# Kernel tuning notes

Measured on AMD Instinct MI355X. Metric: run time of the kernel, lower is better.

Reference implementation:

```python
import jax, jax.numpy as jnp
import numpy as np

N_NODES = 100000
N_EDGES = 600000
D_FEAT = 128
D_DOT = 4


def setup_inputs() -> dict:
    key = jax.random.key(0)
    k1, k2, k3, k4, k5 = jax.random.split(key, 5)
    n = jax.random.normal(k1, (N_NODES, D_FEAT), dtype=jnp.float32)
    e = jax.random.normal(k2, (N_EDGES, D_FEAT), dtype=jnp.float32)
    # xavier_uniform for Linear(D_FEAT, D_DOT); bias filled with 0
    limit = float(np.sqrt(6.0 / (D_FEAT + D_DOT)))
    W = jax.random.uniform(k3, (D_DOT, D_FEAT), dtype=jnp.float32, minval=-limit, maxval=limit)
    b = jnp.zeros((D_DOT,), dtype=jnp.float32)
    src_idx = jax.random.randint(k4, (N_EDGES,), 0, N_NODES, dtype=jnp.int64)
    dst_idx = jax.random.randint(k5, (N_EDGES,), 0, N_NODES, dtype=jnp.int64)
    return {"n": n, "e": e, "W": W, "b": b, "src_idx": src_idx, "dst_idx": dst_idx}


def reference(n, e, W, b, src_idx, dst_idx):
    # gather per-edge src/dst node features: [E, D]
    src = n[src_idx]
    dst = n[dst_idx]
    # include_edge_features=True: mean of node and edge features
    src = (src + e) * 0.5
    dst = (dst + e) * 0.5
    # tiny linear projection to dot_product_dim=4: [E, 4]
    hs = src @ W.T + b
    hd = dst @ W.T + b
    # per-edge dot product (bmm of [E,1,4] x [E,4,1] -> [E,1]) then sigmoid
    score = jax.nn.sigmoid(jnp.sum(hs * hd, axis=-1, keepdims=True))
    return score
```

## Files before the change

### kernel.cpp

```cpp
#include <hip/hip_runtime.h>
#include <math.h>

#define D_FEAT 128
#define D_DOT  4


__device__ __forceinline__ float dot4(const float4 a, const float4 b) {
    return a.x * b.x + a.y * b.y + a.z * b.z + a.w * b.w;
}

template <int CTRL>
__device__ __forceinline__ float dpp_add(float x) {
    union { float f; int i; } u, v;
    u.f = x;
    v.i = __builtin_amdgcn_update_dpp(u.i, u.i, CTRL, 0xF, 0xF, true);
    return x + v.f;
}

__device__ __forceinline__ float row_reduce16(float x) {
    x = dpp_add<0x128>(x);
    x = dpp_add<0x124>(x);
    x = dpp_add<0x122>(x);
    x = dpp_add<0x121>(x);
    return x;
}

__global__ __launch_bounds__(256, 4) void node_proj_kernel(
    const float* __restrict__ n,
    const float* __restrict__ W,
    float* __restrict__ pn,
    int n_nodes)
{
    const int t    = threadIdx.x;
    const int lane = t & 63;
    const int sub  = lane & 15;
    const int g    = lane >> 4;
    const int wave = t >> 6;
    const int base = blockIdx.x * 48 + wave * 12;
    const int last = n_nodes - 1;

    int r[3], c[3];
#pragma unroll
    for (int i = 0; i < 3; ++i) {
        r[i] = base + i * 4 + g;
        c[i] = r[i] > last ? last : r[i];
    }

    const float4* n4 = reinterpret_cast<const float4*>(n);
    float4 xl[3], xh[3];
#pragma unroll
    for (int i = 0; i < 3; ++i) {
        xl[i] = n4[(size_t)c[i] * 32 + sub];
        xh[i] = n4[(size_t)c[i] * 32 + sub + 16];
    }

    const float4* W4 = reinterpret_cast<const float4*>(W);
    float4 wlo[D_DOT], whi[D_DOT];
#pragma unroll
    for (int k = 0; k < D_DOT; ++k) {
        wlo[k] = W4[k * 32 + sub];
        whi[k] = W4[k * 32 + sub + 16];
    }

    float a[3][D_DOT];
#pragma unroll
    for (int i = 0; i < 3; ++i)
#pragma unroll
        for (int k = 0; k < D_DOT; ++k)
            a[i][k] = dot4(xl[i], wlo[k]) + dot4(xh[i], whi[k]);

#pragma unroll
    for (int i = 0; i < 3; ++i)
#pragma unroll
        for (int k = 0; k < D_DOT; ++k)
            a[i][k] = row_reduce16(a[i][k]);

#pragma unroll
    for (int i = 0; i < 3; ++i)
        if (sub == 0 && r[i] < n_nodes)
            reinterpret_cast<float4*>(pn)[r[i]] =
                make_float4(a[i][0], a[i][1], a[i][2], a[i][3]);
}

__global__ __launch_bounds__(256, 4) void edge_score_kernel(
    const float* __restrict__ e,
    const float* __restrict__ W,
    const float* __restrict__ bias,
    const float* __restrict__ pn,
    const int* __restrict__ src_idx,
    const int* __restrict__ dst_idx,
    float* __restrict__ out,
    int n_edges)
{
    const int t    = threadIdx.x;
    const int lane = t & 63;
    const int sub  = lane & 15;
    const int g    = lane >> 4;
    const int wave = t >> 6;
    const int base = blockIdx.x * 48 + wave * 12;
    const int last = n_edges - 1;

    int r[3], c[3];
#pragma unroll
    for (int i = 0; i < 3; ++i) {
        r[i] = base + i * 4 + g;
        c[i] = r[i] > last ? last : r[i];
    }

    int sI[3], dI[3];
#pragma unroll
    for (int i = 0; i < 3; ++i) { sI[i] = src_idx[c[i]]; dI[i] = dst_idx[c[i]]; }

    const float4* e4 = reinterpret_cast<const float4*>(e);
    float4 xl[3], xh[3];
#pragma unroll
    for (int i = 0; i < 3; ++i) {
        xl[i] = e4[(size_t)c[i] * 32 + sub];
        xh[i] = e4[(size_t)c[i] * 32 + sub + 16];
    }

    const float4* W4 = reinterpret_cast<const float4*>(W);
    float4 wlo[D_DOT], whi[D_DOT];
#pragma unroll
    for (int k = 0; k < D_DOT; ++k) {
        wlo[k] = W4[k * 32 + sub];
        whi[k] = W4[k * 32 + sub + 16];
    }
    const float b0 = bias[0], b1 = bias[1], b2 = bias[2], b3 = bias[3];

    const float4* pn4 = reinterpret_cast<const float4*>(pn);
    float4 ps[3], pd[3];
#pragma unroll
    for (int i = 0; i < 3; ++i) { ps[i] = pn4[sI[i]]; pd[i] = pn4[dI[i]]; }

    float a[3][D_DOT];
#pragma unroll
    for (int i = 0; i < 3; ++i)
#pragma unroll
        for (int k = 0; k < D_DOT; ++k)
            a[i][k] = dot4(xl[i], wlo[k]) + dot4(xh[i], whi[k]);

#pragma unroll
    for (int i = 0; i < 3; ++i)
#pragma unroll
        for (int k = 0; k < D_DOT; ++k)
            a[i][k] = row_reduce16(a[i][k]);

#pragma unroll
    for (int i = 0; i < 3; ++i) {
        const float u0 = 0.5f * a[i][0] + b0, u1 = 0.5f * a[i][1] + b1;
        const float u2 = 0.5f * a[i][2] + b2, u3 = 0.5f * a[i][3] + b3;
        const float dot = (0.5f * ps[i].x + u0) * (0.5f * pd[i].x + u0)
                        + (0.5f * ps[i].y + u1) * (0.5f * pd[i].y + u1)
                        + (0.5f * ps[i].z + u2) * (0.5f * pd[i].z + u2)
                        + (0.5f * ps[i].w + u3) * (0.5f * pd[i].w + u3);
        if (sub == 0 && r[i] < n_edges)
            out[r[i]] = 1.0f / (1.0f + __expf(-dot));
    }
}

extern "C" void kernel_launch(void* const* d_in, const int* in_sizes, int n_in,
                              void* d_out, int out_size, void* d_ws, size_t ws_size,
                              hipStream_t stream) {
    const float* n    = (const float*)d_in[0];
    const float* e    = (const float*)d_in[1];
    const float* W    = (const float*)d_in[2];
    const float* bias = (const float*)d_in[3];
    const int*   src  = (const int*)d_in[4];
    const int*   dst  = (const int*)d_in[5];
    float* out = (float*)d_out;

    const int n_nodes = in_sizes[0] / D_FEAT;
    const int n_edges = in_sizes[1] / D_FEAT;

    float* pn = (float*)d_ws;

    const int nblk = (n_nodes + 47) / 48;
    const int eblk = (n_edges + 47) / 48;
    node_proj_kernel<<<nblk, 256, 0, stream>>>(n, W, pn, n_nodes);
    edge_score_kernel<<<eblk, 256, 0, stream>>>(e, W, bias, pn, src, dst, out, n_edges);
}
```

Baseline: 77.78 us.

## Fuse node projection and edge scoring into one cooperative persistent kernel

Replaces the two launches with one cooperative kernel of fixed grid size. It runs grid-stride loops over nodes and then edges, separated by a grid-wide sync, and loads W and bias once per thread. The aim is to remove the second launch and per-block weight reloads. In exchange it adds grid-sync cost and fixes the grid at 1024 blocks, which may underfill or serialize work. It falls back to the old two-kernel path if the cooperative launch fails.

```diff
diff --git a/kernel.cpp b/kernel.cpp
--- a/kernel.cpp
+++ b/kernel.cpp
@@ -1,8 +1,13 @@
 #include <hip/hip_runtime.h>
+#include <hip/hip_cooperative_groups.h>
 #include <math.h>
+
+namespace cg = cooperative_groups;
 
 #define D_FEAT 128
 #define D_DOT  4
+#define NBLK   1024
+#define RPB    48
 
 
 __device__ __forceinline__ float dot4(const float4 a, const float4 b) {
@@ -25,27 +30,136 @@
     return x;
 }
 
-__global__ __launch_bounds__(256, 4) void node_proj_kernel(
+__global__ __launch_bounds__(256, 4) void fused_kernel(
     const float* __restrict__ n,
+    const float* __restrict__ e,
     const float* __restrict__ W,
+    const float* __restrict__ bias,
+    const int* __restrict__ src_idx,
+    const int* __restrict__ dst_idx,
+    float* __restrict__ out,
     float* __restrict__ pn,
-    int n_nodes)
+    int n_nodes, int n_edges)
 {
     const int t    = threadIdx.x;
     const int lane = t & 63;
     const int sub  = lane & 15;
     const int g    = lane >> 4;
     const int wave = t >> 6;
-    const int base = blockIdx.x * 48 + wave * 12;
+
+    const float4* W4 = reinterpret_cast<const float4*>(W);
+    float4 wlo[D_DOT], whi[D_DOT];
+#pragma unroll
+    for (int k = 0; k < D_DOT; ++k) {
+        wlo[k] = W4[k * 32 + sub];
+        whi[k] = W4[k * 32 + sub + 16];
+    }
+    const float b0 = bias[0], b1 = bias[1], b2 = bias[2], b3 = bias[3];
+
+    const int wave_start = blockIdx.x * RPB + wave * 12;
+    const int stride = gridDim.x * RPB;
+
+    {
+        const int last = n_nodes - 1;
+        const float4* n4 = reinterpret_cast<const float4*>(n);
+        for (int base = wave_start; base < n_nodes; base += stride) {
+            int r[3], c[3];
+#pragma unroll
+            for (int i = 0; i < 3; ++i) {
+                r[i] = base + i * 4 + g;
+                c[i] = r[i] > last ? last : r[i];
+            }
+            float4 xl[3], xh[3];
+#pragma unroll
+            for (int i = 0; i < 3; ++i) {
+                xl[i] = n4[(size_t)c[i] * 32 + sub];
+                xh[i] = n4[(size_t)c[i] * 32 + sub + 16];
+            }
+            float a[3][D_DOT];
+#pragma unroll
+            for (int i = 0; i < 3; ++i)
+#pragma unroll
+                for (int k = 0; k < D_DOT; ++k)
+                    a[i][k] = dot4(xl[i], wlo[k]) + dot4(xh[i], whi[k]);
+#pragma unroll
+            for (int i = 0; i < 3; ++i)
+#pragma unroll
+                for (int k = 0; k < D_DOT; ++k)
+                    a[i][k] = row_reduce16(a[i][k]);
+#pragma unroll
+            for (int i = 0; i < 3; ++i)
+                if (sub == 0 && r[i] < n_nodes)
+                    reinterpret_cast<float4*>(pn)[r[i]] =
+                        make_float4(a[i][0], a[i][1], a[i][2], a[i][3]);
+        }
+    }
+
+    __threadfence();
+    cg::this_grid().sync();
+
+    {
+        const int last = n_edges - 1;
+        const float4* e4  = reinterpret_cast<const float4*>(e);
+        const float4* pn4 = reinterpret_cast<const float4*>(pn);
+        for (int base = wave_start; base < n_edges; base += stride) {
+            int r[3], c[3];
+#pragma unroll
+            for (int i = 0; i < 3; ++i) {
+                r[i] = base + i * 4 + g;
+                c[i] = r[i] > last ? last : r[i];
+            }
+            int sI[3], dI[3];
+#pragma unroll
+            for (int i = 0; i < 3; ++i) { sI[i] = src_idx[c[i]]; dI[i] = dst_idx[c[i]]; }
+
+            float4 xl[3], xh[3];
+#pragma unroll
+            for (int i = 0; i < 3; ++i) {
+                xl[i] = e4[(size_t)c[i] * 32 + sub];
+                xh[i] = e4[(size_t)c[i] * 32 + sub + 16];
+            }
+            float4 ps[3], pd[3];
+#pragma unroll
+            for (int i = 0; i < 3; ++i) { ps[i] = pn4[sI[i]]; pd[i] = pn4[dI[i]]; }
+
+            float a[3][D_DOT];
+#pragma unroll
+            for (int i = 0; i < 3; ++i)
+#pragma unroll
+                for (int k = 0; k < D_DOT; ++k)
+                    a[i][k] = dot4(xl[i], wlo[k]) + dot4(xh[i], whi[k]);
+#pragma unroll
+            for (int i = 0; i < 3; ++i)
+#pragma unroll
+                for (int k = 0; k < D_DOT; ++k)
+                    a[i][k] = row_reduce16(a[i][k]);
+
+#pragma unroll
+            for (int i = 0; i < 3; ++i) {
+                const float u0 = 0.5f * a[i][0] + b0, u1 = 0.5f * a[i][1] + b1;
+                const float u2 = 0.5f * a[i][2] + b2, u3 = 0.5f * a[i][3] + b3;
+                const float dot = (0.5f * ps[i].x + u0) * (0.5f * pd[i].x + u0)
+                                + (0.5f * ps[i].y + u1) * (0.5f * pd[i].y + u1)
+                                + (0.5f * ps[i].z + u2) * (0.5f * pd[i].z + u2)
+                                + (0.5f * ps[i].w + u3) * (0.5f * pd[i].w + u3);
+                if (sub == 0 && r[i] < n_edges)
+                    out[r[i]] = 1.0f / (1.0f + __expf(-dot));
+            }
+        }
+    }
+}
+
+__global__ __launch_bounds__(256, 4) void node_proj_kernel(
+    const float* __restrict__ n, const float* __restrict__ W,
+    float* __restrict__ pn, int n_nodes)
+{
+    const int t = threadIdx.x, lane = t & 63, sub = lane & 15, g = lane >> 4;
+    const int wave = t >> 6;
+    const int base = blockIdx.x * RPB + wave * 12;
     const int last = n_nodes - 1;
-
     int r[3], c[3];
 #pragma unroll
-    for (int i = 0; i < 3; ++i) {
-        r[i] = base + i * 4 + g;
-        c[i] = r[i] > last ? last : r[i];
-    }
-
+    for (int i = 0; i < 3; ++i) { r[i] = base + i * 4 + g; c[i] = r[i] > last ? last : r[i]; }
     const float4* n4 = reinterpret_cast<const float4*>(n);
     float4 xl[3], xh[3];
 #pragma unroll
@@ -53,64 +167,43 @@
         xl[i] = n4[(size_t)c[i] * 32 + sub];
         xh[i] = n4[(size_t)c[i] * 32 + sub + 16];
     }
-
     const float4* W4 = reinterpret_cast<const float4*>(W);
     float4 wlo[D_DOT], whi[D_DOT];
 #pragma unroll
-    for (int k = 0; k < D_DOT; ++k) {
-        wlo[k] = W4[k * 32 + sub];
-        whi[k] = W4[k * 32 + sub + 16];
-    }
-
+    for (int k = 0; k < D_DOT; ++k) { wlo[k] = W4[k * 32 + sub]; whi[k] = W4[k * 32 + sub + 16]; }
     float a[3][D_DOT];
 #pragma unroll
     for (int i = 0; i < 3; ++i)
 #pragma unroll
         for (int k = 0; k < D_DOT; ++k)
             a[i][k] = dot4(xl[i], wlo[k]) + dot4(xh[i], whi[k]);
-
 #pragma unroll
     for (int i = 0; i < 3; ++i)
 #pragma unroll
         for (int k = 0; k < D_DOT; ++k)
             a[i][k] = row_reduce16(a[i][k]);
-
 #pragma unroll
     for (int i = 0; i < 3; ++i)
         if (sub == 0 && r[i] < n_nodes)
-            reinterpret_cast<float4*>(pn)[r[i]] =
-                make_float4(a[i][0], a[i][1], a[i][2], a[i][3]);
+            reinterpret_cast<float4*>(pn)[r[i]] = make_float4(a[i][0], a[i][1], a[i][2], a[i][3]);
 }
 
 __global__ __launch_bounds__(256, 4) void edge_score_kernel(
-    const float* __restrict__ e,
-    const float* __restrict__ W,
-    const float* __restrict__ bias,
-    const float* __restrict__ pn,
-    const int* __restrict__ src_idx,
-    const int* __restrict__ dst_idx,
-    float* __restrict__ out,
-    int n_edges)
+    const float* __restrict__ e, const float* __restrict__ W,
+    const float* __restrict__ bias, const float* __restrict__ pn,
+    const int* __restrict__ src_idx, const int* __restrict__ dst_idx,
+    float* __restrict__ out, int n_edges)
 {
-    const int t    = threadIdx.x;
-    const int lane = t & 63;
-    const int sub  = lane & 15;
-    const int g    = lane >> 4;
+    const int t = threadIdx.x, lane = t & 63, sub = lane & 15, g = lane >> 4;
     const int wave = t >> 6;
-    const int base = blockIdx.x * 48 + wave * 12;
+    const int base = blockIdx.x * RPB + wave * 12;
     const int last = n_edges - 1;
-
     int r[3], c[3];
 #pragma unroll
-    for (int i = 0; i < 3; ++i) {
-        r[i] = base + i * 4 + g;
-        c[i] = r[i] > last ? last : r[i];
-    }
-
+    for (int i = 0; i < 3; ++i) { r[i] = base + i * 4 + g; c[i] = r[i] > last ? last : r[i]; }
     int sI[3], dI[3];
 #pragma unroll
     for (int i = 0; i < 3; ++i) { sI[i] = src_idx[c[i]]; dI[i] = dst_idx[c[i]]; }
-
     const float4* e4 = reinterpret_cast<const float4*>(e);
     float4 xl[3], xh[3];
 #pragma unroll
@@ -118,34 +211,26 @@
         xl[i] = e4[(size_t)c[i] * 32 + sub];
         xh[i] = e4[(size_t)c[i] * 32 + sub + 16];
     }
-
     const float4* W4 = reinterpret_cast<const float4*>(W);
     float4 wlo[D_DOT], whi[D_DOT];
 #pragma unroll
-    for (int k = 0; k < D_DOT; ++k) {
-        wlo[k] = W4[k * 32 + sub];
-        whi[k] = W4[k * 32 + sub + 16];
-    }
+    for (int k = 0; k < D_DOT; ++k) { wlo[k] = W4[k * 32 + sub]; whi[k] = W4[k * 32 + sub + 16]; }
     const float b0 = bias[0], b1 = bias[1], b2 = bias[2], b3 = bias[3];
-
     const float4* pn4 = reinterpret_cast<const float4*>(pn);
     float4 ps[3], pd[3];
 #pragma unroll
     for (int i = 0; i < 3; ++i) { ps[i] = pn4[sI[i]]; pd[i] = pn4[dI[i]]; }
-
     float a[3][D_DOT];
 #pragma unroll
     for (int i = 0; i < 3; ++i)
 #pragma unroll
         for (int k = 0; k < D_DOT; ++k)
             a[i][k] = dot4(xl[i], wlo[k]) + dot4(xh[i], whi[k]);
-
 #pragma unroll
     for (int i = 0; i < 3; ++i)
 #pragma unroll
         for (int k = 0; k < D_DOT; ++k)
             a[i][k] = row_reduce16(a[i][k]);
-
 #pragma unroll
     for (int i = 0; i < 3; ++i) {
         const float u0 = 0.5f * a[i][0] + b0, u1 = 0.5f * a[i][1] + b1;
@@ -170,13 +255,21 @@
     const int*   dst  = (const int*)d_in[5];
     float* out = (float*)d_out;
 
-    const int n_nodes = in_sizes[0] / D_FEAT;
-    const int n_edges = in_sizes[1] / D_FEAT;
+    int n_nodes = in_sizes[0] / D_FEAT;
+    int n_edges = in_sizes[1] / D_FEAT;
 
     float* pn = (float*)d_ws;
 
-    const int nblk = (n_nodes + 47) / 48;
-    const int eblk = (n_edges + 47) / 48;
-    node_proj_kernel<<<nblk, 256, 0, stream>>>(n, W, pn, n_nodes);
-    edge_score_kernel<<<eblk, 256, 0, stream>>>(e, W, bias, pn, src, dst, out, n_edges);
-}
+    void* args[] = {(void*)&n, (void*)&e, (void*)&W, (void*)&bias,
+                    (void*)&src, (void*)&dst, (void*)&out, (void*)&pn,
+                    (void*)&n_nodes, (void*)&n_edges};
+    hipError_t err = hipLaunchCooperativeKernel((const void*)fused_kernel,
+                                                dim3(NBLK), dim3(256),
+                                                args, 0, stream);
+    if (err != hipSuccess) {
+        const int nblk = (n_nodes + RPB - 1) / RPB;
+        const int eblk = (n_edges + RPB - 1) / RPB;
+        node_proj_kernel<<<nblk, 256, 0, stream>>>(n, W, pn, n_nodes);
+        edge_score_kernel<<<eblk, 256, 0, stream>>>(e, W, bias, pn, src, dst, out, n_edges);
+    }
+}
```

After: 297.1 us. +282.0%, slower.
